# Kernel tuning notes

Measured on AMD Instinct MI355X. Metric: run time of the kernel, lower is better.

## Reference

```python
import jax, jax.numpy as jnp
import numpy as np

N = 262144  # number of points
W = 256     # feature width


def setup_inputs() -> dict:
    key = jax.random.key(0)
    k1, k2, k3 = jax.random.split(key, 3)
    x = jax.random.normal(k1, (N, W), dtype=jnp.float32)
    # torch nn.Linear(W, 9) layout: weight [out, in], bias [out]
    fc_w = jax.random.normal(k2, (9, W), dtype=jnp.float32) * (1.0 / np.sqrt(W))
    fc_b = jax.random.normal(k3, (9,), dtype=jnp.float32) * 0.01
    return {"x": x, "fc_w": fc_w, "fc_b": fc_b}


def symmetric_orthogonalization(m):
    # m: [n, 3, 3] -> nearest rotation matrix (special orthogonal Procrustes)
    u, s, vt = jnp.linalg.svd(m, full_matrices=False)
    det = jnp.linalg.det(jnp.einsum('nij,njk->nik', u, vt))  # [n]
    ones = jnp.ones_like(det)
    d = jnp.stack([ones, ones, det], axis=-1)  # [n, 3] diag(1, 1, det)
    r = jnp.einsum('nij,nj,njk->nik', u, d, vt)
    return r


def reference(x, fc_w, fc_b):
    # x: [N, W] -> rotations flattened to [N, 9] (out_type='mat', out_rots=1)
    y = x @ fc_w.T + fc_b            # [N, 9]
    m = y.reshape(-1, 3, 3)          # [N, 3, 3]
    r = symmetric_orthogonalization(m)
    return r.reshape(x.shape[:-1] + (9,))
```

## Files before the change

### kernel.cpp

```cpp
#include <hip/hip_runtime.h>
#include <math.h>

#define N_PTS 262144
#define WIDTH 256

__device__ __forceinline__ void jrot(float &app, float &aqq, float &apq,
                                     float &arp, float &arq,
                                     float &vp0, float &vq0,
                                     float &vp1, float &vq1,
                                     float &vp2, float &vq2)
{
    float a = apq;
    if (fabsf(a) < 1e-20f) return;
    float theta = (aqq - app) / (2.0f * a);
    float tt = copysignf(1.0f, theta) / (fabsf(theta) + sqrtf(1.0f + theta * theta));
    float c = 1.0f / sqrtf(1.0f + tt * tt);
    float s = tt * c;
    app -= tt * a;
    aqq += tt * a;
    apq = 0.0f;
    float rp = arp, rq = arq;
    arp = c * rp - s * rq;
    arq = s * rp + c * rq;
    float t0p = vp0, t0q = vq0; vp0 = c * t0p - s * t0q; vq0 = s * t0p + c * t0q;
    float t1p = vp1, t1q = vq1; vp1 = c * t1p - s * t1q; vq1 = s * t1p + c * t1q;
    float t2p = vp2, t2q = vq2; vp2 = c * t2p - s * t2q; vq2 = s * t2p + c * t2q;
}

__global__ __launch_bounds__(256, 4) void so3_kernel(
    const float* __restrict__ x,
    const float* __restrict__ fw,
    const float* __restrict__ fb,
    float* __restrict__ out)
{
    __shared__ float xs[4][64][33];
    const int lane = threadIdx.x & 63;
    const int w    = threadIdx.x >> 6;
    const int r0   = (((blockIdx.x << 2) + w) << 6);
    float (*tile)[33] = xs[w];

    const int a = lane >> 3;
    const int b = lane & 7;

    float y[9];
#pragma unroll
    for (int j = 0; j < 9; ++j) y[j] = 0.f;

    float4 pre[8];
#pragma unroll
    for (int i = 0; i < 8; ++i) {
        const int row = (i << 3) + a;
        pre[i] = *reinterpret_cast<const float4*>(
            x + (size_t)(r0 + row) * WIDTH + (b << 2));
    }

    for (int kc = 0; kc < 8; ++kc) {
#pragma unroll
        for (int i = 0; i < 8; ++i) {
            const int row = (i << 3) + a;
            const int c   = b << 2;
            tile[row][c + 0] = pre[i].x;
            tile[row][c + 1] = pre[i].y;
            tile[row][c + 2] = pre[i].z;
            tile[row][c + 3] = pre[i].w;
        }

        if (kc < 7) {
            const int k0n = (kc + 1) << 5;
#pragma unroll
            for (int i = 0; i < 8; ++i) {
                const int row = (i << 3) + a;
                pre[i] = *reinterpret_cast<const float4*>(
                    x + (size_t)(r0 + row) * WIDTH + k0n + (b << 2));
            }
        }

        const int k0 = kc << 5;
#pragma unroll
        for (int kk = 0; kk < 32; ++kk) {
            const float xv = tile[lane][kk];
            const int k = k0 + kk;
#pragma unroll
            for (int j = 0; j < 9; ++j)
                y[j] = fmaf(xv, fw[j * WIDTH + k], y[j]);
        }
    }

#pragma unroll
    for (int j = 0; j < 9; ++j) y[j] += fb[j];

    const float m00 = y[0], m01 = y[1], m02 = y[2];
    const float m10 = y[3], m11 = y[4], m12 = y[5];
    const float m20 = y[6], m21 = y[7], m22 = y[8];

    float a00 = m00*m00 + m10*m10 + m20*m20;
    float a01 = m00*m01 + m10*m11 + m20*m21;
    float a02 = m00*m02 + m10*m12 + m20*m22;
    float a11 = m01*m01 + m11*m11 + m21*m21;
    float a12 = m01*m02 + m11*m12 + m21*m22;
    float a22 = m02*m02 + m12*m12 + m22*m22;

    float v[3][3] = { {1,0,0}, {0,1,0}, {0,0,1} };

#pragma unroll
    for (int sw = 0; sw < 5; ++sw) {
        jrot(a00, a11, a01, a02, a12,
             v[0][0], v[0][1], v[1][0], v[1][1], v[2][0], v[2][1]);
        jrot(a00, a22, a02, a01, a12,
             v[0][0], v[0][2], v[1][0], v[1][2], v[2][0], v[2][2]);
        jrot(a11, a22, a12, a01, a02,
             v[0][1], v[0][2], v[1][1], v[1][2], v[2][1], v[2][2]);
    }

    float d0 = a00, d1 = a11, d2 = a22, tmp;
    if (d0 < d1) { tmp=d0; d0=d1; d1=tmp;
        tmp=v[0][0]; v[0][0]=v[0][1]; v[0][1]=tmp;
        tmp=v[1][0]; v[1][0]=v[1][1]; v[1][1]=tmp;
        tmp=v[2][0]; v[2][0]=v[2][1]; v[2][1]=tmp; }
    if (d0 < d2) { tmp=d0; d0=d2; d2=tmp;
        tmp=v[0][0]; v[0][0]=v[0][2]; v[0][2]=tmp;
        tmp=v[1][0]; v[1][0]=v[1][2]; v[1][2]=tmp;
        tmp=v[2][0]; v[2][0]=v[2][2]; v[2][2]=tmp; }
    if (d1 < d2) { tmp=d1; d1=d2; d2=tmp;
        tmp=v[0][1]; v[0][1]=v[0][2]; v[0][2]=tmp;
        tmp=v[1][1]; v[1][1]=v[1][2]; v[1][2]=tmp;
        tmp=v[2][1]; v[2][1]=v[2][2]; v[2][2]=tmp; }

    const float v1x = v[0][0], v1y = v[1][0], v1z = v[2][0];
    const float v2x = v[0][1], v2y = v[1][1], v2z = v[2][1];

    float u1x = m00*v1x + m01*v1y + m02*v1z;
    float u1y = m10*v1x + m11*v1y + m12*v1z;
    float u1z = m20*v1x + m21*v1y + m22*v1z;
    float inv1 = 1.0f / (sqrtf(u1x*u1x + u1y*u1y + u1z*u1z) + 1e-30f);
    u1x *= inv1; u1y *= inv1; u1z *= inv1;

    float u2x = m00*v2x + m01*v2y + m02*v2z;
    float u2y = m10*v2x + m11*v2y + m12*v2z;
    float u2z = m20*v2x + m21*v2y + m22*v2z;
    const float d12 = u1x*u2x + u1y*u2y + u1z*u2z;
    u2x -= d12*u1x; u2y -= d12*u1y; u2z -= d12*u1z;
    float inv2 = 1.0f / (sqrtf(u2x*u2x + u2y*u2y + u2z*u2z) + 1e-30f);
    u2x *= inv2; u2y *= inv2; u2z *= inv2;

    const float u3x = u1y*u2z - u1z*u2y;
    const float u3y = u1z*u2x - u1x*u2z;
    const float u3z = u1x*u2y - u1y*u2x;
    const float v3x = v1y*v2z - v1z*v2y;
    const float v3y = v1z*v2x - v1x*v2z;
    const float v3z = v1x*v2y - v1y*v2x;

    float r[9];
    r[0] = u1x*v1x + u2x*v2x + u3x*v3x;
    r[1] = u1x*v1y + u2x*v2y + u3x*v3y;
    r[2] = u1x*v1z + u2x*v2z + u3x*v3z;
    r[3] = u1y*v1x + u2y*v2x + u3y*v3x;
    r[4] = u1y*v1y + u2y*v2y + u3y*v3y;
    r[5] = u1y*v1z + u2y*v2z + u3y*v3z;
    r[6] = u1z*v1x + u2z*v2x + u3z*v3x;
    r[7] = u1z*v1y + u2z*v2y + u3z*v3y;
    r[8] = u1z*v1z + u2z*v2z + u3z*v3z;

    float* o = out + (size_t)(r0 + lane) * 9;
#pragma unroll
    for (int j = 0; j < 9; ++j) o[j] = r[j];
}

extern "C" void kernel_launch(void* const* d_in, const int* in_sizes, int n_in,
                              void* d_out, int out_size, void* d_ws, size_t ws_size,
                              hipStream_t stream) {
    const float* x  = (const float*)d_in[0];
    const float* fw = (const float*)d_in[1];
    const float* fb = (const float*)d_in[2];
    float* out = (float*)d_out;
    dim3 grid(N_PTS / 256), block(256);
    hipLaunchKernelGGL(so3_kernel, grid, block, 0, stream, x, fw, fb, out);
}
```

Baseline: 68.39 us.

## Split the feature dimension across two wavefronts per row group with a shared-memory reduction

Each group of 64 rows is now handled by two wavefronts, each covering half of the 256-wide feature dimension. Partial dot products are combined through shared memory after a block barrier. Launch bounds rise to 8 blocks per multiprocessor and the grid doubles, aiming for more parallelism and memory-level concurrency on this bandwidth-bound projection. The cost is a block barrier and a redundant SVD epilogue, since half the lanes compute results that are never stored.

```diff
diff --git a/kernel.cpp b/kernel.cpp
--- a/kernel.cpp
+++ b/kernel.cpp
@@ -27,37 +27,41 @@
     float t2p = vp2, t2q = vq2; vp2 = c * t2p - s * t2q; vq2 = s * t2p + c * t2q;
 }
 
-__global__ __launch_bounds__(256, 4) void so3_kernel(
+__global__ __launch_bounds__(256, 8) void so3_kernel(
     const float* __restrict__ x,
     const float* __restrict__ fw,
     const float* __restrict__ fb,
     float* __restrict__ out)
 {
-    __shared__ float xs[4][64][33];
-    const int lane = threadIdx.x & 63;
-    const int w    = threadIdx.x >> 6;
-    const int r0   = (((blockIdx.x << 2) + w) << 6);
-    float (*tile)[33] = xs[w];
+    __shared__ float xs[4][64][17];
+    const int tid  = threadIdx.x;
+    const int lane = tid & 63;
+    const int w    = tid >> 6;
+    const int pair = w >> 1;
+    const int h    = w & 1;
+    const int r0   = ((blockIdx.x << 1) + pair) << 6;
+    const int cb   = h << 7;
+    float (*tile)[17] = xs[w];
 
-    const int a = lane >> 3;
-    const int b = lane & 7;
+    const int a = lane >> 2;
+    const int b = lane & 3;
 
     float y[9];
 #pragma unroll
     for (int j = 0; j < 9; ++j) y[j] = 0.f;
 
-    float4 pre[8];
+    float4 pre[4];
 #pragma unroll
-    for (int i = 0; i < 8; ++i) {
-        const int row = (i << 3) + a;
+    for (int i = 0; i < 4; ++i) {
+        const int row = (i << 4) + a;
         pre[i] = *reinterpret_cast<const float4*>(
-            x + (size_t)(r0 + row) * WIDTH + (b << 2));
+            x + (size_t)(r0 + row) * WIDTH + cb + (b << 2));
     }
 
     for (int kc = 0; kc < 8; ++kc) {
 #pragma unroll
-        for (int i = 0; i < 8; ++i) {
-            const int row = (i << 3) + a;
+        for (int i = 0; i < 4; ++i) {
+            const int row = (i << 4) + a;
             const int c   = b << 2;
             tile[row][c + 0] = pre[i].x;
             tile[row][c + 1] = pre[i].y;
@@ -66,18 +70,18 @@
         }
 
         if (kc < 7) {
-            const int k0n = (kc + 1) << 5;
+            const int k0n = cb + ((kc + 1) << 4);
 #pragma unroll
-            for (int i = 0; i < 8; ++i) {
-                const int row = (i << 3) + a;
+            for (int i = 0; i < 4; ++i) {
+                const int row = (i << 4) + a;
                 pre[i] = *reinterpret_cast<const float4*>(
                     x + (size_t)(r0 + row) * WIDTH + k0n + (b << 2));
             }
         }
 
-        const int k0 = kc << 5;
+        const int k0 = cb + (kc << 4);
 #pragma unroll
-        for (int kk = 0; kk < 32; ++kk) {
+        for (int kk = 0; kk < 16; ++kk) {
             const float xv = tile[lane][kk];
             const int k = k0 + kk;
 #pragma unroll
@@ -87,11 +91,21 @@
     }
 
 #pragma unroll
-    for (int j = 0; j < 9; ++j) y[j] += fb[j];
+    for (int j = 0; j < 9; ++j) tile[lane][j] = y[j];
+    __syncthreads();
 
-    const float m00 = y[0], m01 = y[1], m02 = y[2];
-    const float m10 = y[3], m11 = y[4], m12 = y[5];
-    const float m20 = y[6], m21 = y[7], m22 = y[8];
+    const int p2 = (h << 5) + (lane & 31);
+    float (*tA)[17] = xs[(pair << 1) + 0];
+    float (*tB)[17] = xs[(pair << 1) + 1];
+
+    float z[9];
+#pragma unroll
+    for (int j = 0; j < 9; ++j)
+        z[j] = tA[p2][j] + tB[p2][j] + fb[j];
+
+    const float m00 = z[0], m01 = z[1], m02 = z[2];
+    const float m10 = z[3], m11 = z[4], m12 = z[5];
+    const float m20 = z[6], m21 = z[7], m22 = z[8];
 
     float a00 = m00*m00 + m10*m10 + m20*m20;
     float a01 = m00*m01 + m10*m11 + m20*m21;
@@ -161,9 +175,11 @@
     r[7] = u1z*v1y + u2z*v2y + u3z*v3y;
     r[8] = u1z*v1z + u2z*v2z + u3z*v3z;
 
-    float* o = out + (size_t)(r0 + lane) * 9;
+    if ((lane & 32) == 0) {
+        float* o = out + (size_t)(r0 + p2) * 9;
 #pragma unroll
-    for (int j = 0; j < 9; ++j) o[j] = r[j];
+        for (int j = 0; j < 9; ++j) o[j] = r[j];
+    }
 }
 
 extern "C" void kernel_launch(void* const* d_in, const int* in_sizes, int n_in,
@@ -173,6 +189,6 @@
     const float* fw = (const float*)d_in[1];
     const float* fb = (const float*)d_in[2];
     float* out = (float*)d_out;
-    dim3 grid(N_PTS / 256), block(256);
+    dim3 grid(N_PTS / 128), block(256);
     hipLaunchKernelGGL(so3_kernel, grid, block, 0, stream, x, fw, fb, out);
 }
```

New measurement: 163.0 us. 138% more time.
